# Kernel tuning notes

Measured on AMD Instinct MI355X. Metric: run time of the kernel, lower is better.

The kernel has to match this reference:

```python
import jax, jax.numpy as jnp
import numpy as np

MUL_S, MUL_V = 256, 128              # 256x0e + 128x1o hidden irreps
DIM_H = MUL_S + 3 * MUL_V            # 640
N_NODES = 100000
INV_SQRT3 = 3.0 ** -0.5
# e3nn 'element' path normalization: sqrt(ir_out.dim / sum_paths(mul1*mul2));
# for the 1o output the extra sqrt(3) cancels the 1/sqrt(3) of the wigner-3j,
# so every path ends up with the same constant.
C0 = (1.0 / (MUL_S + MUL_V)) ** 0.5


def _unif(key, shape, fan):
    # matches linear_layer_init: uniform(-a, a), a = sqrt(6/(mul1*mul2 + mul_out)), mul2 = 1
    a = (6.0 / fan) ** 0.5
    return jax.random.uniform(key, shape, minval=-a, maxval=a, dtype=jnp.float32)


def setup_inputs() -> dict:
    key = jax.random.key(0)
    ks = jax.random.split(key, 8)
    data_in = jax.random.normal(ks[0], (N_NODES, DIM_H + 4), dtype=jnp.float32)
    return {
        "data_in": data_in,
        "W_ss": _unif(ks[1], (MUL_S, MUL_S), MUL_S + MUL_S),      # 0e x 0e -> 0e (scalars)
        "W_vv": _unif(ks[2], (MUL_V, MUL_S), MUL_V + MUL_S),      # 1o x 1o -> 0e (scalars)
        "W_ss_g": _unif(ks[3], (MUL_S, MUL_V), MUL_S + MUL_V),    # 0e x 0e -> 0e (gates)
        "W_vv_g": _unif(ks[4], (MUL_V, MUL_V), MUL_V + MUL_V),    # 1o x 1o -> 0e (gates)
        "W_sv": _unif(ks[5], (MUL_S, MUL_V), MUL_S + MUL_V),      # 0e x 1o -> 1o
        "W_vs": _unif(ks[6], (MUL_V, MUL_V), MUL_V + MUL_V),      # 1o x 0e -> 1o
        "b": jnp.zeros((MUL_S,), dtype=jnp.float32),
    }


def reference(data_in, W_ss, W_vv, W_ss_g, W_vv_g, W_sv, W_vs, b):
    # split hidden / pos parts (forward does data_in[:, :-irreps_pos.dim] etc.)
    xs = data_in[:, :MUL_S]                           # [N, 256] 0e
    xv = data_in[:, MUL_S:DIM_H].reshape(-1, MUL_V, 3)  # [N, 128, 3] 1o
    ps = data_in[:, DIM_H:DIM_H + 1]                  # [N, 1] pos scalar
    pv = data_in[:, DIM_H + 1:]                       # [N, 3] pos vector

    # CG invariants feeding the 0e outputs
    s0 = xs * ps                                       # 0e x 0e path
    dot = jnp.einsum('nuk,nk->nu', xv, pv) * INV_SQRT3  # 1o x 1o -> 0e path, [N, 128]

    scal = C0 * (s0 @ W_ss + dot @ W_vv) + b           # [N, 256] scalars (+bias on N_trivial)
    gate = C0 * (s0 @ W_ss_g + dot @ W_vv_g)           # [N, 128] gates

    # 1o outputs: 0e x 1o and 1o x 0e paths
    v1 = (xs @ W_sv)[:, :, None] * pv[:, None, :]            # [N, 128, 3]
    v2 = jnp.einsum('nuk,uw->nwk', xv, W_vs) * ps[:, :, None]  # [N, 128, 3]
    vec = C0 * (v1 + v2)

    # Gate: Swish(beta=1) on scalars, sigmoid(gates) multiplying gated 1o irreps
    scal_out = scal * jax.nn.sigmoid(scal)
    vec_out = vec * jax.nn.sigmoid(gate)[:, :, None]
    return jnp.concatenate([scal_out, vec_out.reshape(-1, 3 * MUL_V)], axis=1)  # [N, 640]
```

## Files before the change

kernel.cpp:

```cpp
#include <hip/hip_runtime.h>
#include <hip/hip_bf16.h>

#define MUL_Sc 256
#define MUL_Vc 128
#define DIM_Hc 640
#define IN_COLS 644
#define KFEAT 1024
#define NT 32

#define C0F 0.05103103630798287f
#define INV_SQRT3F 0.57735026918962576f

typedef __attribute__((ext_vector_type(8))) short short8;
typedef __attribute__((ext_vector_type(4))) float f32x4;

#define MFMA(a, b, c) __builtin_amdgcn_mfma_f32_16x16x32_bf16((a), (b), (c), 0, 0, 0)

__device__ __forceinline__ unsigned short f2bf(float x) {
    union { float f; unsigned u; } v; v.f = x;
    unsigned r = v.u + 0x7fffu + ((v.u >> 16) & 1u);
    return (unsigned short)(r >> 16);
}
__device__ __forceinline__ float bf2f(unsigned short h) {
    union { unsigned u; float f; } v; v.u = ((unsigned)h) << 16;
    return v.f;
}

__global__ void prep_weights(const float* __restrict__ Wss, const float* __restrict__ Wvv,
                             const float* __restrict__ Wssg, const float* __restrict__ Wvvg,
                             const float* __restrict__ Wsv, const float* __restrict__ Wvs,
                             unsigned short* __restrict__ wt) {
    int i = blockIdx.x * 256 + threadIdx.x;
    const int N_SG = 384 * 384;
    const int N_SV = 128 * 256;
    const int N_VS = 128 * 128;
    if (i < N_SG) {
        int col = i / 384, k = i % 384;
        float v;
        if (col < 256) v = (k < 256) ? Wss[k * 256 + col] : Wvv[(k - 256) * 256 + col];
        else { int c = col - 256; v = (k < 256) ? Wssg[k * 128 + c] : Wvvg[(k - 256) * 128 + c]; }
        wt[i] = f2bf(v);
    } else if (i < N_SG + N_SV) {
        int j = i - N_SG; int col = j >> 8, k = j & 255;
        wt[i] = f2bf(Wsv[k * 128 + col]);
    } else if (i < N_SG + N_SV + N_VS) {
        int j = i - N_SG - N_SV; int col = j >> 7, k = j & 127;
        wt[i] = f2bf(Wvs[k * 128 + col]);
    }
}

__global__ __launch_bounds__(512, 4)
void fused_main(const float* __restrict__ din, const unsigned short* __restrict__ wt,
                const float* __restrict__ bias, float* __restrict__ out, int N) {
    __shared__ unsigned short feat[NT * KFEAT];
    __shared__ unsigned short sgate[NT * MUL_Vc];
    __shared__ float psv[NT * 4];

    const int tid = threadIdx.x;
    const int n0 = blockIdx.x * NT;

    {
        const int g = tid >> 4;
        const int j = tid & 15;
        int n = n0 + g; if (n >= N) n = N - 1;
        const float* row = din + (size_t)n * IN_COLS;
        float ps  = row[DIM_Hc];
        float pv0 = row[DIM_Hc + 1], pv1 = row[DIM_Hc + 2], pv2 = row[DIM_Hc + 3];
        if (j == 0) { psv[g*4+0] = ps; psv[g*4+1] = pv0; psv[g*4+2] = pv1; psv[g*4+3] = pv2; }
        char* fb = (char*)feat;
        const int swz  = (g & 7) << 4;
        const int rowb = g * (KFEAT * 2);
        #pragma unroll
        for (int it = 0; it < 8; ++it) {
            int c = 2 * j + 32 * it;
            float2 x = *(const float2*)(row + c);
            unsigned xsp = (unsigned)f2bf(x.x)      | ((unsigned)f2bf(x.y)      << 16);
            unsigned s0p = (unsigned)f2bf(x.x * ps) | ((unsigned)f2bf(x.y * ps) << 16);
            *(unsigned*)(fb + ((rowb + c * 2) ^ swz))         = s0p;
            *(unsigned*)(fb + ((rowb + (384 + c) * 2) ^ swz)) = xsp;
        }
        #pragma unroll
        for (int it = 0; it < 4; ++it) {
            int u = 2 * j + 32 * it;
            const float* p = row + MUL_Sc + 3 * u;
            float a0 = p[0], a1 = p[1], a2 = p[2], b0 = p[3], b1 = p[4], b2 = p[5];
            float d0 = (a0 * pv0 + a1 * pv1 + a2 * pv2) * INV_SQRT3F;
            float d1 = (b0 * pv0 + b1 * pv1 + b2 * pv2) * INV_SQRT3F;
            *(unsigned*)(fb + ((rowb + (256 + u) * 2) ^ swz)) = (unsigned)f2bf(d0) | ((unsigned)f2bf(d1) << 16);
            *(unsigned*)(fb + ((rowb + (640 + u) * 2) ^ swz)) = (unsigned)f2bf(a0) | ((unsigned)f2bf(b0) << 16);
            *(unsigned*)(fb + ((rowb + (768 + u) * 2) ^ swz)) = (unsigned)f2bf(a1) | ((unsigned)f2bf(b1) << 16);
            *(unsigned*)(fb + ((rowb + (896 + u) * 2) ^ swz)) = (unsigned)f2bf(a2) | ((unsigned)f2bf(b2) << 16);
        }
    }
    __syncthreads();

    const int wave = tid >> 6;
    const int lane = tid & 63;
    const int l15  = lane & 15;
    const int lkb  = (lane >> 4) << 3;
    const char* fbr = (const char*)feat;
    const int swzr = (l15 & 7) << 4;

    const unsigned short* WTsg = wt;
    const unsigned short* WTsv = wt + 384 * 384;
    const unsigned short* WTvs = wt + 384 * 384 + 128 * 256;

    f32x4 accS[3][2];
    #pragma unroll
    for (int t = 0; t < 3; ++t) { accS[t][0] = (f32x4){0,0,0,0}; accS[t][1] = (f32x4){0,0,0,0}; }

    #pragma unroll
    for (int ks = 0; ks < 12; ++ks) {
        int kf = ks * 32 + lkb;
        short8 a0 = *(const short8*)(fbr + (((0  + l15) * 2048 + kf * 2) ^ swzr));
        short8 a1 = *(const short8*)(fbr + (((16 + l15) * 2048 + kf * 2) ^ swzr));
        #pragma unroll
        for (int t = 0; t < 3; ++t) {
            int ct = wave + t * 8;
            short8 b = *(const short8*)(WTsg + (ct * 16 + l15) * 384 + ks * 32 + lkb);
            accS[t][0] = MFMA(a0, b, accS[t][0]);
            accS[t][1] = MFMA(a1, b, accS[t][1]);
        }
    }
    {
        const int rbase = (lane >> 4) << 2;
        #pragma unroll
        for (int t = 0; t < 3; ++t) {
            int ct = wave + t * 8;
            int col = ct * 16 + l15;
            if (ct < 16) {
                float bc = bias[col];
                #pragma unroll
                for (int s = 0; s < 2; ++s)
                #pragma unroll
                for (int i = 0; i < 4; ++i) {
                    int nl = s * 16 + rbase + i;
                    int n = n0 + nl;
                    if (n < N) {
                        float sc = C0F * accS[t][s][i] + bc;
                        out[(size_t)n * DIM_Hc + col] = sc / (1.f + __expf(-sc));
                    }
                }
            } else {
                int gc = col - 256;
                #pragma unroll
                for (int s = 0; s < 2; ++s)
                #pragma unroll
                for (int i = 0; i < 4; ++i) {
                    int nl = s * 16 + rbase + i;
                    float gt = C0F * accS[t][s][i];
                    sgate[nl * MUL_Vc + gc] = f2bf(1.f / (1.f + __expf(-gt)));
                }
            }
        }
    }

    f32x4 accA[2], accV[3][2];
    accA[0] = (f32x4){0,0,0,0}; accA[1] = (f32x4){0,0,0,0};
    #pragma unroll
    for (int k = 0; k < 3; ++k) { accV[k][0] = (f32x4){0,0,0,0}; accV[k][1] = (f32x4){0,0,0,0}; }
    const int ut = wave;

    #pragma unroll
    for (int ks = 0; ks < 8; ++ks) {
        short8 b = *(const short8*)(WTsv + (ut * 16 + l15) * 256 + ks * 32 + lkb);
        int kf = 384 + ks * 32 + lkb;
        short8 a0 = *(const short8*)(fbr + (((0  + l15) * 2048 + kf * 2) ^ swzr));
        short8 a1 = *(const short8*)(fbr + (((16 + l15) * 2048 + kf * 2) ^ swzr));
        accA[0] = MFMA(a0, b, accA[0]);
        accA[1] = MFMA(a1, b, accA[1]);
    }
    #pragma unroll
    for (int ks = 0; ks < 4; ++ks) {
        short8 b = *(const short8*)(WTvs + (ut * 16 + l15) * 128 + ks * 32 + lkb);
        #pragma unroll
        for (int k = 0; k < 3; ++k) {
            int kf = 640 + 128 * k + ks * 32 + lkb;
            short8 a0 = *(const short8*)(fbr + (((0  + l15) * 2048 + kf * 2) ^ swzr));
            short8 a1 = *(const short8*)(fbr + (((16 + l15) * 2048 + kf * 2) ^ swzr));
            accV[k][0] = MFMA(a0, b, accV[k][0]);
            accV[k][1] = MFMA(a1, b, accV[k][1]);
        }
    }
    __syncthreads();

    {
        const int rbase = (lane >> 4) << 2;
        int u = ut * 16 + l15;
        #pragma unroll
        for (int s = 0; s < 2; ++s)
        #pragma unroll
        for (int i = 0; i < 4; ++i) {
            int nl = s * 16 + rbase + i;
            int n = n0 + nl;
            if (n >= N) continue;
            float sg  = bf2f(sgate[nl * MUL_Vc + u]);
            float ps  = psv[nl * 4 + 0];
            float pv0 = psv[nl * 4 + 1], pv1 = psv[nl * 4 + 2], pv2 = psv[nl * 4 + 3];
            float av = accA[s][i];
            size_t ob = (size_t)n * DIM_Hc + MUL_Sc + 3 * u;
            out[ob + 0] = C0F * (av * pv0 + accV[0][s][i] * ps) * sg;
            out[ob + 1] = C0F * (av * pv1 + accV[1][s][i] * ps) * sg;
            out[ob + 2] = C0F * (av * pv2 + accV[2][s][i] * ps) * sg;
        }
    }
}

extern "C" void kernel_launch(void* const* d_in, const int* in_sizes, int n_in,
                              void* d_out, int out_size, void* d_ws, size_t ws_size,
                              hipStream_t stream) {
    const float* din  = (const float*)d_in[0];
    const float* Wss  = (const float*)d_in[1];
    const float* Wvv  = (const float*)d_in[2];
    const float* Wssg = (const float*)d_in[3];
    const float* Wvvg = (const float*)d_in[4];
    const float* Wsv  = (const float*)d_in[5];
    const float* Wvs  = (const float*)d_in[6];
    const float* bias = (const float*)d_in[7];
    float* out = (float*)d_out;
    unsigned short* wt = (unsigned short*)d_ws;

    const size_t WT_BYTES = (size_t)(384 * 384 + 128 * 256 + 128 * 128) * 2;
    if (ws_size < WT_BYTES) return;

    int N = in_sizes[0] / IN_COLS;

    int prep_total = 384 * 384 + 128 * 256 + 128 * 128;
    prep_weights<<<(prep_total + 255) / 256, 256, 0, stream>>>(Wss, Wvv, Wssg, Wvvg, Wsv, Wvs, wt);

    int nblocks = (N + NT - 1) / NT;
    fused_main<<<nblocks, 512, 0, stream>>>(din, wt, bias, out, N);
}
```

Before: 237.1 us.

## Halve node tile to 16 rows and vectorise input staging loads

Shrinks the per-block node tile from 32 to 16 so each wave does one MFMA row-tile instead of two, and raises the occupancy hint to 8 blocks per CU. Staging of input rows into shared memory now uses float4 loads and wider bf16 vector stores. This aims to raise occupancy and latency hiding and reduce LDS use per block, but it halves reuse of each weight fragment loaded from global memory, doubling weight traffic per node.

```diff
diff --git a/kernel.cpp b/kernel.cpp
--- a/kernel.cpp
+++ b/kernel.cpp
@@ -6,12 +6,13 @@
 #define DIM_Hc 640
 #define IN_COLS 644
 #define KFEAT 1024
-#define NT 32
+#define NT 16
 
 #define C0F 0.05103103630798287f
 #define INV_SQRT3F 0.57735026918962576f
 
 typedef __attribute__((ext_vector_type(8))) short short8;
+typedef __attribute__((ext_vector_type(4))) short bf16x4_t;
 typedef __attribute__((ext_vector_type(4))) float f32x4;
 
 #define MFMA(a, b, c) __builtin_amdgcn_mfma_f32_16x16x32_bf16((a), (b), (c), 0, 0, 0)
@@ -49,7 +50,7 @@
     }
 }
 
-__global__ __launch_bounds__(512, 4)
+__global__ __launch_bounds__(512, 8)
 void fused_main(const float* __restrict__ din, const unsigned short* __restrict__ wt,
                 const float* __restrict__ bias, float* __restrict__ out, int N) {
     __shared__ unsigned short feat[NT * KFEAT];
@@ -60,8 +61,8 @@
     const int n0 = blockIdx.x * NT;
 
     {
-        const int g = tid >> 4;
-        const int j = tid & 15;
+        const int g = tid >> 5;
+        const int j = tid & 31;
         int n = n0 + g; if (n >= N) n = N - 1;
         const float* row = din + (size_t)n * IN_COLS;
         float ps  = row[DIM_Hc];
@@ -70,26 +71,38 @@
         char* fb = (char*)feat;
         const int swz  = (g & 7) << 4;
         const int rowb = g * (KFEAT * 2);
-        #pragma unroll
-        for (int it = 0; it < 8; ++it) {
-            int c = 2 * j + 32 * it;
-            float2 x = *(const float2*)(row + c);
-            unsigned xsp = (unsigned)f2bf(x.x)      | ((unsigned)f2bf(x.y)      << 16);
-            unsigned s0p = (unsigned)f2bf(x.x * ps) | ((unsigned)f2bf(x.y * ps) << 16);
-            *(unsigned*)(fb + ((rowb + c * 2) ^ swz))         = s0p;
-            *(unsigned*)(fb + ((rowb + (384 + c) * 2) ^ swz)) = xsp;
-        }
-        #pragma unroll
-        for (int it = 0; it < 4; ++it) {
-            int u = 2 * j + 32 * it;
-            const float* p = row + MUL_Sc + 3 * u;
-            float a0 = p[0], a1 = p[1], a2 = p[2], b0 = p[3], b1 = p[4], b2 = p[5];
-            float d0 = (a0 * pv0 + a1 * pv1 + a2 * pv2) * INV_SQRT3F;
-            float d1 = (b0 * pv0 + b1 * pv1 + b2 * pv2) * INV_SQRT3F;
-            *(unsigned*)(fb + ((rowb + (256 + u) * 2) ^ swz)) = (unsigned)f2bf(d0) | ((unsigned)f2bf(d1) << 16);
-            *(unsigned*)(fb + ((rowb + (640 + u) * 2) ^ swz)) = (unsigned)f2bf(a0) | ((unsigned)f2bf(b0) << 16);
-            *(unsigned*)(fb + ((rowb + (768 + u) * 2) ^ swz)) = (unsigned)f2bf(a1) | ((unsigned)f2bf(b1) << 16);
-            *(unsigned*)(fb + ((rowb + (896 + u) * 2) ^ swz)) = (unsigned)f2bf(a2) | ((unsigned)f2bf(b2) << 16);
+
+        {
+            int c = 8 * j;
+            float4 x0 = *(const float4*)(row + c);
+            float4 x1 = *(const float4*)(row + c + 4);
+            short8 s0p, xsp;
+            s0p[0]=(short)f2bf(x0.x*ps); s0p[1]=(short)f2bf(x0.y*ps); s0p[2]=(short)f2bf(x0.z*ps); s0p[3]=(short)f2bf(x0.w*ps);
+            s0p[4]=(short)f2bf(x1.x*ps); s0p[5]=(short)f2bf(x1.y*ps); s0p[6]=(short)f2bf(x1.z*ps); s0p[7]=(short)f2bf(x1.w*ps);
+            xsp[0]=(short)f2bf(x0.x); xsp[1]=(short)f2bf(x0.y); xsp[2]=(short)f2bf(x0.z); xsp[3]=(short)f2bf(x0.w);
+            xsp[4]=(short)f2bf(x1.x); xsp[5]=(short)f2bf(x1.y); xsp[6]=(short)f2bf(x1.z); xsp[7]=(short)f2bf(x1.w);
+            *(short8*)(fb + ((rowb + c * 2) ^ swz))         = s0p;
+            *(short8*)(fb + ((rowb + (384 + c) * 2) ^ swz)) = xsp;
+        }
+        {
+            int u0 = 4 * j;
+            const float* p = row + MUL_Sc + 3 * u0;
+            float4 q0 = *(const float4*)(p);
+            float4 q1 = *(const float4*)(p + 4);
+            float4 q2 = *(const float4*)(p + 8);
+            float d0 = (q0.x*pv0 + q0.y*pv1 + q0.z*pv2) * INV_SQRT3F;
+            float d1 = (q0.w*pv0 + q1.x*pv1 + q1.y*pv2) * INV_SQRT3F;
+            float d2 = (q1.z*pv0 + q1.w*pv1 + q2.x*pv2) * INV_SQRT3F;
+            float d3 = (q2.y*pv0 + q2.z*pv1 + q2.w*pv2) * INV_SQRT3F;
+            bf16x4_t dp, k0, k1, k2;
+            dp[0]=(short)f2bf(d0); dp[1]=(short)f2bf(d1); dp[2]=(short)f2bf(d2); dp[3]=(short)f2bf(d3);
+            k0[0]=(short)f2bf(q0.x); k0[1]=(short)f2bf(q0.w); k0[2]=(short)f2bf(q1.z); k0[3]=(short)f2bf(q2.y);
+            k1[0]=(short)f2bf(q0.y); k1[1]=(short)f2bf(q1.x); k1[2]=(short)f2bf(q1.w); k1[3]=(short)f2bf(q2.z);
+            k2[0]=(short)f2bf(q0.z); k2[1]=(short)f2bf(q1.y); k2[2]=(short)f2bf(q2.x); k2[3]=(short)f2bf(q2.w);
+            *(bf16x4_t*)(fb + ((rowb + (256 + u0) * 2) ^ swz)) = dp;
+            *(bf16x4_t*)(fb + ((rowb + (640 + u0) * 2) ^ swz)) = k0;
+            *(bf16x4_t*)(fb + ((rowb + (768 + u0) * 2) ^ swz)) = k1;
+            *(bf16x4_t*)(fb + ((rowb + (896 + u0) * 2) ^ swz)) = k2;
         }
     }
     __syncthreads();
@@ -105,21 +118,19 @@
     const unsigned short* WTsv = wt + 384 * 384;
     const unsigned short* WTvs = wt + 384 * 384 + 128 * 256;
 
-    f32x4 accS[3][2];
-    #pragma unroll
-    for (int t = 0; t < 3; ++t) { accS[t][0] = (f32x4){0,0,0,0}; accS[t][1] = (f32x4){0,0,0,0}; }
+    f32x4 accS[3];
+    #pragma unroll
+    for (int t = 0; t < 3; ++t) accS[t] = (f32x4){0,0,0,0};
 
     #pragma unroll
     for (int ks = 0; ks < 12; ++ks) {
         int kf = ks * 32 + lkb;
-        short8 a0 = *(const short8*)(fbr + (((0  + l15) * 2048 + kf * 2) ^ swzr));
-        short8 a1 = *(const short8*)(fbr + (((16 + l15) * 2048 + kf * 2) ^ swzr));
+        short8 a = *(const short8*)(fbr + ((l15 * 2048 + kf * 2) ^ swzr));
         #pragma unroll
         for (int t = 0; t < 3; ++t) {
             int ct = wave + t * 8;
             short8 b = *(const short8*)(WTsg + (ct * 16 + l15) * 384 + ks * 32 + lkb);
-            accS[t][0] = MFMA(a0, b, accS[t][0]);
-            accS[t][1] = MFMA(a1, b, accS[t][1]);
+            accS[t] = MFMA(a, b, accS[t]);
         }
     }
     {
@@ -131,44 +142,38 @@
             if (ct < 16) {
                 float bc = bias[col];
                 #pragma unroll
-                for (int s = 0; s < 2; ++s)
-                #pragma unroll
                 for (int i = 0; i < 4; ++i) {
-                    int nl = s * 16 + rbase + i;
+                    int nl = rbase + i;
                     int n = n0 + nl;
                     if (n < N) {
-                        float sc = C0F * accS[t][s][i] + bc;
+                        float sc = C0F * accS[t][i] + bc;
                         out[(size_t)n * DIM_Hc + col] = sc / (1.f + __expf(-sc));
                     }
                 }
             } else {
                 int gc = col - 256;
                 #pragma unroll
-                for (int s = 0; s < 2; ++s)
-                #pragma unroll
                 for (int i = 0; i < 4; ++i) {
-                    int nl = s * 16 + rbase + i;
-                    float gt = C0F * accS[t][s][i];
+                    int nl = rbase + i;
+                    float gt = C0F * accS[t][i];
                     sgate[nl * MUL_Vc + gc] = f2bf(1.f / (1.f + __expf(-gt)));
                 }
             }
         }
     }
 
-    f32x4 accA[2], accV[3][2];
-    accA[0] = (f32x4){0,0,0,0}; accA[1] = (f32x4){0,0,0,0};
-    #pragma unroll
-    for (int k = 0; k < 3; ++k) { accV[k][0] = (f32x4){0,0,0,0}; accV[k][1] = (f32x4){0,0,0,0}; }
+    f32x4 accA, accV[3];
+    accA = (f32x4){0,0,0,0};
+    #pragma unroll
+    for (int k = 0; k < 3; ++k) accV[k] = (f32x4){0,0,0,0};
     const int ut = wave;
 
     #pragma unroll
     for (int ks = 0; ks < 8; ++ks) {
         short8 b = *(const short8*)(WTsv + (ut * 16 + l15) * 256 + ks * 32 + lkb);
         int kf = 384 + ks * 32 + lkb;
-        short8 a0 = *(const short8*)(fbr + (((0  + l15) * 2048 + kf * 2) ^ swzr));
-        short8 a1 = *(const short8*)(fbr + (((16 + l15) * 2048 + kf * 2) ^ swzr));
-        accA[0] = MFMA(a0, b, accA[0]);
-        accA[1] = MFMA(a1, b, accA[1]);
+        short8 a = *(const short8*)(fbr + ((l15 * 2048 + kf * 2) ^ swzr));
+        accA = MFMA(a, b, accA);
     }
     #pragma unroll
     for (int ks = 0; ks < 4; ++ks) {
@@ -176,10 +181,8 @@
         #pragma unroll
         for (int k = 0; k < 3; ++k) {
             int kf = 640 + 128 * k + ks * 32 + lkb;
-            short8 a0 = *(const short8*)(fbr + (((0  + l15) * 2048 + kf * 2) ^ swzr));
-            short8 a1 = *(const short8*)(fbr + (((16 + l15) * 2048 + kf * 2) ^ swzr));
-            accV[k][0] = MFMA(a0, b, accV[k][0]);
-            accV[k][1] = MFMA(a1, b, accV[k][1]);
+            short8 a = *(const short8*)(fbr + ((l15 * 2048 + kf * 2) ^ swzr));
+            accV[k] = MFMA(a, b, accV[k]);
         }
     }
     __syncthreads();
@@ -188,20 +191,18 @@
         const int rbase = (lane >> 4) << 2;
         int u = ut * 16 + l15;
         #pragma unroll
-        for (int s = 0; s < 2; ++s)
-        #pragma unroll
         for (int i = 0; i < 4; ++i) {
-            int nl = s * 16 + rbase + i;
+            int nl = rbase + i;
             int n = n0 + nl;
             if (n >= N) continue;
             float sg  = bf2f(sgate[nl * MUL_Vc + u]);
             float ps  = psv[nl * 4 + 0];
             float pv0 = psv[nl * 4 + 1], pv1 = psv[nl * 4 + 2], pv2 = psv[nl * 4 + 3];
-            float av = accA[s][i];
+            float av = accA[i];
             size_t ob = (size_t)n * DIM_Hc + MUL_Sc + 3 * u;
-            out[ob + 0] = C0F * (av * pv0 + accV[0][s][i] * ps) * sg;
-            out[ob + 1] = C0F * (av * pv1 + accV[1][s][i] * ps) * sg;
-            out[ob + 2] = C0F * (av * pv2 + accV[2][s][i] * ps) * sg;
+            out[ob + 0] = C0F * (av * pv0 + accV[0][i] * ps) * sg;
+            out[ob + 1] = C0F * (av * pv1 + accV[1][i] * ps) * sg;
+            out[ob + 2] = C0F * (av * pv2 + accV[2][i] * ps) * sg;
         }
     }
 }
```

Result: slower. 327.7 us (+38.2%).

## Factor ps out of scalar GEMM, shrink LDS feature tile, prefetch weights, vectorize staging

Applied to the files above, without the earlier changes.

The s0 = xs*ps features are no longer stored. The GEMM over the raw xs columns is kept in a separate accumulator, and ps is applied per row afterwards, which cuts the shared-memory feature tile from 1024 to 768 columns. The gate buffer is dropped and gates are written back into the now-dead dot region of the feature tile after a barrier. Staging now uses float4 loads and short8 stores, and the weight B fragments are double-buffered from global memory. This lowers LDS footprint and store traffic, but adds an extra barrier and reorders bf16 rounding (ps is now applied in fp32 after the bf16 product).

```diff
diff --git a/kernel.cpp b/kernel.cpp
--- a/kernel.cpp
+++ b/kernel.cpp
@@ -5,7 +5,7 @@
 #define MUL_Vc 128
 #define DIM_Hc 640
 #define IN_COLS 644
-#define KFEAT 1024
+#define KF 768
 #define NT 32
 
 #define C0F 0.05103103630798287f
@@ -52,8 +52,7 @@
 __global__ __launch_bounds__(512, 4)
 void fused_main(const float* __restrict__ din, const unsigned short* __restrict__ wt,
                 const float* __restrict__ bias, float* __restrict__ out, int N) {
-    __shared__ unsigned short feat[NT * KFEAT];
-    __shared__ unsigned short sgate[NT * MUL_Vc];
+    __shared__ unsigned short feat[NT * KF];
     __shared__ float psv[NT * 4];
 
     const int tid = threadIdx.x;
@@ -69,27 +68,44 @@
         if (j == 0) { psv[g*4+0] = ps; psv[g*4+1] = pv0; psv[g*4+2] = pv1; psv[g*4+3] = pv2; }
         char* fb = (char*)feat;
         const int swz  = (g & 7) << 4;
-        const int rowb = g * (KFEAT * 2);
-        #pragma unroll
-        for (int it = 0; it < 8; ++it) {
-            int c = 2 * j + 32 * it;
-            float2 x = *(const float2*)(row + c);
-            unsigned xsp = (unsigned)f2bf(x.x)      | ((unsigned)f2bf(x.y)      << 16);
-            unsigned s0p = (unsigned)f2bf(x.x * ps) | ((unsigned)f2bf(x.y * ps) << 16);
-            *(unsigned*)(fb + ((rowb + c * 2) ^ swz))         = s0p;
-            *(unsigned*)(fb + ((rowb + (384 + c) * 2) ^ swz)) = xsp;
-        }
-        #pragma unroll
-        for (int it = 0; it < 4; ++it) {
-            int u = 2 * j + 32 * it;
-            const float* p = row + MUL_Sc + 3 * u;
-            float a0 = p[0], a1 = p[1], a2 = p[2], b0 = p[3], b1 = p[4], b2 = p[5];
-            float d0 = (a0 * pv0 + a1 * pv1 + a2 * pv2) * INV_SQRT3F;
-            float d1 = (b0 * pv0 + b1 * pv1 + b2 * pv2) * INV_SQRT3F;
-            *(unsigned*)(fb + ((rowb + (256 + u) * 2) ^ swz)) = (unsigned)f2bf(d0) | ((unsigned)f2bf(d1) << 16);
-            *(unsigned*)(fb + ((rowb + (640 + u) * 2) ^ swz)) = (unsigned)f2bf(a0) | ((unsigned)f2bf(b0) << 16);
-            *(unsigned*)(fb + ((rowb + (768 + u) * 2) ^ swz)) = (unsigned)f2bf(a1) | ((unsigned)f2bf(b1) << 16);
-            *(unsigned*)(fb + ((rowb + (896 + u) * 2) ^ swz)) = (unsigned)f2bf(a2) | ((unsigned)f2bf(b2) << 16);
+        const int rowb = g * (KF * 2);
+
+        {
+            int c = 16 * j;
+            float4 x0 = *(const float4*)(row + c);
+            float4 x1 = *(const float4*)(row + c + 4);
+            float4 x2 = *(const float4*)(row + c + 8);
+            float4 x3 = *(const float4*)(row + c + 12);
+            short8 p0, p1;
+            p0[0]=(short)f2bf(x0.x); p0[1]=(short)f2bf(x0.y); p0[2]=(short)f2bf(x0.z); p0[3]=(short)f2bf(x0.w);
+            p0[4]=(short)f2bf(x1.x); p0[5]=(short)f2bf(x1.y); p0[6]=(short)f2bf(x1.z); p0[7]=(short)f2bf(x1.w);
+            p1[0]=(short)f2bf(x2.x); p1[1]=(short)f2bf(x2.y); p1[2]=(short)f2bf(x2.z); p1[3]=(short)f2bf(x2.w);
+            p1[4]=(short)f2bf(x3.x); p1[5]=(short)f2bf(x3.y); p1[6]=(short)f2bf(x3.z); p1[7]=(short)f2bf(x3.w);
+            *(short8*)(fb + ((rowb + c * 2) ^ swz))       = p0;
+            *(short8*)(fb + ((rowb + (c + 8) * 2) ^ swz)) = p1;
+        }
+        {
+            int u0 = 8 * j;
+            const float* p = row + MUL_Sc + 3 * u0;
+            float e[24];
+            #pragma unroll
+            for (int q = 0; q < 6; ++q) {
+                float4 v = *(const float4*)(p + 4 * q);
+                e[4*q+0] = v.x; e[4*q+1] = v.y; e[4*q+2] = v.z; e[4*q+3] = v.w;
+            }
+            short8 dp, k0, k1, k2;
+            #pragma unroll
+            for (int m = 0; m < 8; ++m) {
+                float a = e[3*m], b = e[3*m+1], c = e[3*m+2];
+                dp[m] = (short)f2bf((a * pv0 + b * pv1 + c * pv2) * INV_SQRT3F);
+                k0[m] = (short)f2bf(a);
+                k1[m] = (short)f2bf(b);
+                k2[m] = (short)f2bf(c);
+            }
+            *(short8*)(fb + ((rowb + (256 + u0) * 2) ^ swz)) = dp;
+            *(short8*)(fb + ((rowb + (384 + u0) * 2) ^ swz)) = k0;
+            *(short8*)(fb + ((rowb + (512 + u0) * 2) ^ swz)) = k1;
+            *(short8*)(fb + ((rowb + (640 + u0) * 2) ^ swz)) = k2;
         }
     }
     __syncthreads();
@@ -105,88 +121,116 @@
     const unsigned short* WTsv = wt + 384 * 384;
     const unsigned short* WTvs = wt + 384 * 384 + 128 * 256;
 
-    f32x4 accS[3][2];
-    #pragma unroll
-    for (int t = 0; t < 3; ++t) { accS[t][0] = (f32x4){0,0,0,0}; accS[t][1] = (f32x4){0,0,0,0}; }
-
+    f32x4 acc1[3][2], acc2[3][2];
+    #pragma unroll
+    for (int t = 0; t < 3; ++t) {
+        acc1[t][0] = (f32x4){0,0,0,0}; acc1[t][1] = (f32x4){0,0,0,0};
+        acc2[t][0] = (f32x4){0,0,0,0}; acc2[t][1] = (f32x4){0,0,0,0};
+    }
+    const unsigned short* bp0 = WTsg + ((wave     ) * 16 + l15) * 384 + lkb;
+    const unsigned short* bp1 = WTsg + ((wave +  8) * 16 + l15) * 384 + lkb;
+    const unsigned short* bp2 = WTsg + ((wave + 16) * 16 + l15) * 384 + lkb;
+    short8 b0a = *(const short8*)(bp0);      short8 b0b = *(const short8*)(bp0 + 32);
+    short8 b1a = *(const short8*)(bp1);      short8 b1b = *(const short8*)(bp1 + 32);
+    short8 b2a = *(const short8*)(bp2);      short8 b2b = *(const short8*)(bp2 + 32);
     #pragma unroll
     for (int ks = 0; ks < 12; ++ks) {
         int kf = ks * 32 + lkb;
-        short8 a0 = *(const short8*)(fbr + (((0  + l15) * 2048 + kf * 2) ^ swzr));
-        short8 a1 = *(const short8*)(fbr + (((16 + l15) * 2048 + kf * 2) ^ swzr));
-        #pragma unroll
-        for (int t = 0; t < 3; ++t) {
-            int ct = wave + t * 8;
-            short8 b = *(const short8*)(WTsg + (ct * 16 + l15) * 384 + ks * 32 + lkb);
-            accS[t][0] = MFMA(a0, b, accS[t][0]);
-            accS[t][1] = MFMA(a1, b, accS[t][1]);
-        }
-    }
+        short8 a0 = *(const short8*)(fbr + ((l15 * 1536 + kf * 2) ^ swzr));
+        short8 a1 = *(const short8*)(fbr + (((16 + l15) * 1536 + kf * 2) ^ swzr));
+        short8 c0 = b0a, c1 = b1a, c2 = b2a;
+        b0a = b0b; b1a = b1b; b2a = b2b;
+        if (ks < 10) {
+            b0b = *(const short8*)(bp0 + (ks + 2) * 32);
+            b1b = *(const short8*)(bp1 + (ks + 2) * 32);
+            b2b = *(const short8*)(bp2 + (ks + 2) * 32);
+        }
+        if (ks < 8) {
+            acc1[0][0] = MFMA(a0, c0, acc1[0][0]); acc1[0][1] = MFMA(a1, c0, acc1[0][1]);
+            acc1[1][0] = MFMA(a0, c1, acc1[1][0]); acc1[1][1] = MFMA(a1, c1, acc1[1][1]);
+            acc1[2][0] = MFMA(a0, c2, acc1[2][0]); acc1[2][1] = MFMA(a1, c2, acc1[2][1]);
+        } else {
+            acc2[0][0] = MFMA(a0, c0, acc2[0][0]); acc2[0][1] = MFMA(a1, c0, acc2[0][1]);
+            acc2[1][0] = MFMA(a0, c1, acc2[1][0]); acc2[1][1] = MFMA(a1, c1, acc2[1][1]);
+            acc2[2][0] = MFMA(a0, c2, acc2[2][0]); acc2[2][1] = MFMA(a1, c2, acc2[2][1]);
+        }
+    }
+    __syncthreads();
+
+    f32x4 accA[2], accV[3][2];
+    accA[0] = (f32x4){0,0,0,0}; accA[1] = (f32x4){0,0,0,0};
+    #pragma unroll
+    for (int k = 0; k < 3; ++k) { accV[k][0] = (f32x4){0,0,0,0}; accV[k][1] = (f32x4){0,0,0,0}; }
+
+    const unsigned short* pA = WTsv + (wave * 16 + l15) * 256 + lkb;
+    const unsigned short* pV = WTvs + (wave * 16 + l15) * 128 + lkb;
+    short8 va = *(const short8*)(pA);      short8 vb = *(const short8*)(pA + 32);
+    #pragma unroll
+    for (int ks = 0; ks < 8; ++ks) {
+        int kf = ks * 32 + lkb;
+        short8 a0 = *(const short8*)(fbr + ((l15 * 1536 + kf * 2) ^ swzr));
+        short8 a1 = *(const short8*)(fbr + (((16 + l15) * 1536 + kf * 2) ^ swzr));
+        short8 cur = va; va = vb;
+        if (ks < 6) vb = *(const short8*)(pA + (ks + 2) * 32);
+        accA[0] = MFMA(a0, cur, accA[0]);
+        accA[1] = MFMA(a1, cur, accA[1]);
+    }
+    short8 wa = *(const short8*)(pV);      short8 wb = *(const short8*)(pV + 32);
+    #pragma unroll
+    for (int ks = 0; ks < 4; ++ks) {
+        short8 cur = wa; wa = wb;
+        if (ks < 2) wb = *(const short8*)(pV + (ks + 2) * 32);
+        #pragma unroll
+        for (int k = 0; k < 3; ++k) {
+            int kf = 384 + 128 * k + ks * 32 + lkb;
+            short8 a0 = *(const short8*)(fbr + ((l15 * 1536 + kf * 2) ^ swzr));
+            short8 a1 = *(const short8*)(fbr + (((16 + l15) * 1536 + kf * 2) ^ swzr));
+            accV[k][0] = MFMA(a0, cur, accV[k][0]);
+            accV[k][1] = MFMA(a1, cur, accV[k][1]);
+        }
+    }
+
     {
         const int rbase = (lane >> 4) << 2;
-        #pragma unroll
-        for (int t = 0; t < 3; ++t) {
-            int ct = wave + t * 8;
-            int col = ct * 16 + l15;
-            if (ct < 16) {
-                float bc = bias[col];
-                #pragma unroll
-                for (int s = 0; s < 2; ++s)
-                #pragma unroll
-                for (int i = 0; i < 4; ++i) {
-                    int nl = s * 16 + rbase + i;
-                    int n = n0 + nl;
-                    if (n < N) {
-                        float sc = C0F * accS[t][s][i] + bc;
-                        out[(size_t)n * DIM_Hc + col] = sc / (1.f + __expf(-sc));
-                    }
-                }
-            } else {
-                int gc = col - 256;
-                #pragma unroll
-                for (int s = 0; s < 2; ++s)
-                #pragma unroll
-                for (int i = 0; i < 4; ++i) {
-                    int nl = s * 16 + rbase + i;
-                    float gt = C0F * accS[t][s][i];
-                    sgate[nl * MUL_Vc + gc] = f2bf(1.f / (1.f + __expf(-gt)));
+        float pss[2][4];
+        #pragma unroll
+        for (int s = 0; s < 2; ++s)
+        #pragma unroll
+        for (int i = 0; i < 4; ++i) pss[s][i] = psv[(s * 16 + rbase + i) * 4];
+
+        #pragma unroll
+        for (int t = 0; t < 2; ++t) {
+            int col = (wave + t * 8) * 16 + l15;
+            float bc = bias[col];
+            #pragma unroll
+            for (int s = 0; s < 2; ++s)
+            #pragma unroll
+            for (int i = 0; i < 4; ++i) {
+                int nl = s * 16 + rbase + i;
+                int n = n0 + nl;
+                if (n < N) {
+                    float sc = C0F * (pss[s][i] * acc1[t][s][i] + acc2[t][s][i]) + bc;
+                    out[(size_t)n * DIM_Hc + col] = sc / (1.f + __expf(-sc));
                 }
             }
         }
-    }
-
-    f32x4 accA[2], accV[3][2];
-    accA[0] = (f32x4){0,0,0,0}; accA[1] = (f32x4){0,0,0,0};
-    #pragma unroll
-    for (int k = 0; k < 3; ++k) { accV[k][0] = (f32x4){0,0,0,0}; accV[k][1] = (f32x4){0,0,0,0}; }
-    const int ut = wave;
-
-    #pragma unroll
-    for (int ks = 0; ks < 8; ++ks) {
-        short8 b = *(const short8*)(WTsv + (ut * 16 + l15) * 256 + ks * 32 + lkb);
-        int kf = 384 + ks * 32 + lkb;
-        short8 a0 = *(const short8*)(fbr + (((0  + l15) * 2048 + kf * 2) ^ swzr));
-        short8 a1 = *(const short8*)(fbr + (((16 + l15) * 2048 + kf * 2) ^ swzr));
-        accA[0] = MFMA(a0, b, accA[0]);
-        accA[1] = MFMA(a1, b, accA[1]);
-    }
-    #pragma unroll
-    for (int ks = 0; ks < 4; ++ks) {
-        short8 b = *(const short8*)(WTvs + (ut * 16 + l15) * 128 + ks * 32 + lkb);
-        #pragma unroll
-        for (int k = 0; k < 3; ++k) {
-            int kf = 640 + 128 * k + ks * 32 + lkb;
-            short8 a0 = *(const short8*)(fbr + (((0  + l15) * 2048 + kf * 2) ^ swzr));
-            short8 a1 = *(const short8*)(fbr + (((16 + l15) * 2048 + kf * 2) ^ swzr));
-            accV[k][0] = MFMA(a0, b, accV[k][0]);
-            accV[k][1] = MFMA(a1, b, accV[k][1]);
+        char* fbw = (char*)feat;
+        int gc = wave * 16 + l15;
+        #pragma unroll
+        for (int s = 0; s < 2; ++s)
+        #pragma unroll
+        for (int i = 0; i < 4; ++i) {
+            int nl = s * 16 + rbase + i;
+            float gt = C0F * (pss[s][i] * acc1[2][s][i] + acc2[2][s][i]);
+            unsigned short sg = f2bf(1.f / (1.f + __expf(-gt)));
+            *(unsigned short*)(fbw + ((nl * 1536 + (256 + gc) * 2) ^ ((nl & 7) << 4))) = sg;
         }
     }
     __syncthreads();
 
     {
         const int rbase = (lane >> 4) << 2;
-        int u = ut * 16 + l15;
+        int u = wave * 16 + l15;
         #pragma unroll
         for (int s = 0; s < 2; ++s)
         #pragma unroll
@@ -194,7 +238,7 @@
             int nl = s * 16 + rbase + i;
             int n = n0 + nl;
             if (n >= N) continue;
-            float sg  = bf2f(sgate[nl * MUL_Vc + u]);
+            float sg  = bf2f(*(const unsigned short*)(fbr + ((nl * 1536 + (256 + u) * 2) ^ ((nl & 7) << 4))));
             float ps  = psv[nl * 4 + 0];
             float pv0 = psv[nl * 4 + 1], pv1 = psv[nl * 4 + 2], pv2 = psv[nl * 4 + 3];
             float av = accA[s][i];
```

Measured after the change: 244.7 us. +3.2%, slower.
